# Performance work log

Hardware: AMD Instinct MI355X
Metric: run time of the kernel (lower is better)

## Reference

```python
import jax, jax.numpy as jnp
import numpy as np

DIM = 512
HEADS = 8
DIM_HEAD = 64
INNER = HEADS * DIM_HEAD
SCALE = DIM_HEAD ** -0.5


def setup_inputs() -> dict:
    key = jax.random.key(0)
    ks = jax.random.split(key, 6)
    b, n = 2, 2048
    x = jax.random.normal(ks[0], (b, n, DIM), dtype=jnp.float32)
    # torch Linear(dim, 3*inner, bias=False): store as [in, out] for x @ W
    w_qkv = jax.random.normal(ks[1], (DIM, 3 * INNER), dtype=jnp.float32) * (DIM ** -0.5)
    # Conv2d(heads, heads, 1, bias=False) weights squeezed to [out_h, in_h]
    w_pre = jax.random.normal(ks[2], (HEADS, HEADS), dtype=jnp.float32) * (HEADS ** -0.5)
    w_post = jax.random.normal(ks[3], (HEADS, HEADS), dtype=jnp.float32) * (HEADS ** -0.5)
    w_out = jax.random.normal(ks[4], (INNER, DIM), dtype=jnp.float32) * (INNER ** -0.5)
    b_out = jax.random.normal(ks[5], (DIM,), dtype=jnp.float32) * 0.01
    return {"x": x, "w_qkv": w_qkv, "w_pre": w_pre, "w_post": w_post,
            "w_out": w_out, "b_out": b_out}


def reference(x, w_qkv, w_pre, w_post, w_out, b_out):
    b, n, _ = x.shape
    qkv = x @ w_qkv  # [b, n, 3*inner]
    q, k, v = jnp.split(qkv, 3, axis=-1)
    # b n (h d) -> b h n d
    split_heads = lambda t: t.reshape(b, n, HEADS, DIM_HEAD).transpose(0, 2, 1, 3)
    q, k, v = split_heads(q), split_heads(k), split_heads(v)
    dots = jnp.einsum('bhid,bhjd->bhij', q, k) * SCALE
    # pre-softmax talking-heads: 1x1 conv over the head axis
    dots = jnp.einsum('gh,bhij->bgij', w_pre, dots)
    attn = jax.nn.softmax(dots, axis=-1)
    # post-softmax talking-heads mix
    attn = jnp.einsum('gh,bhij->bgij', w_post, attn)
    out = jnp.einsum('bhij,bhjd->bhid', attn, v)
    out = out.transpose(0, 2, 1, 3).reshape(b, n, INNER)  # b h n d -> b n (h d)
    return out @ w_out + b_out
```

## Files before the change

### kernel.cpp

```cpp
#include <hip/hip_runtime.h>
#include <hip/hip_bf16.h>

typedef unsigned short ushort_t;
typedef __attribute__((ext_vector_type(8))) short short8;
typedef __attribute__((ext_vector_type(4))) short short4v;
typedef __attribute__((ext_vector_type(4))) float floatx4;

#define MFMA16(a, b, c) __builtin_amdgcn_mfma_f32_16x16x32_bf16(a, b, c, 0, 0, 0)

__device__ __forceinline__ float bf2f(ushort_t u) {
    unsigned int v = ((unsigned int)u) << 16;
    return __int_as_float((int)v);
}
__device__ __forceinline__ ushort_t f2bf(float f) {
    unsigned int x = (unsigned int)__float_as_int(f);
    unsigned int r = (x + 0x7FFFu + ((x >> 16) & 1u)) >> 16;
    return (ushort_t)r;
}

__global__ __launch_bounds__(256) void k_cvt(const floatx4* __restrict__ src,
                                             short4v* __restrict__ dst, int n4) {
    int i = blockIdx.x * 256 + threadIdx.x;
    if (i < n4) {
        floatx4 v = src[i];
        short4v o;
        o[0] = (short)f2bf(v[0]);
        o[1] = (short)f2bf(v[1]);
        o[2] = (short)f2bf(v[2]);
        o[3] = (short)f2bf(v[3]);
        dst[i] = o;
    }
}

__global__ __launch_bounds__(256) void k_transpose_cvt(const float* __restrict__ src,
                                                       ushort_t* __restrict__ dst, int R, int C) {
    __shared__ float t[32][33];
    int tx = threadIdx.x & 31, ty = threadIdx.x >> 5;
    int r0 = blockIdx.y * 32, c0 = blockIdx.x * 32;
    for (int y = ty; y < 32; y += 8) t[y][tx] = src[(r0 + y) * C + c0 + tx];
    __syncthreads();
    for (int y = ty; y < 32; y += 8) dst[(c0 + y) * R + r0 + tx] = f2bf(t[tx][y]);
}

__global__ __launch_bounds__(256) void k_qkv(const ushort_t* __restrict__ x,
                                             const ushort_t* __restrict__ wt,
                                             ushort_t* __restrict__ qs,
                                             ushort_t* __restrict__ ks,
                                             ushort_t* __restrict__ vt) {
    __shared__ __align__(16) ushort_t st[64 * 72];
    const int tid = threadIdx.x, lane = tid & 63, wv = tid >> 6;
    const int col = lane & 15, quad = lane >> 4;
    const int row0 = blockIdx.y * 64 + (wv >> 1) * 32;
    const int c0 = blockIdx.x * 64 + (wv & 1) * 32;
    const int which = blockIdx.x >> 3, hh = blockIdx.x & 7;
    const int brow0 = blockIdx.y * 64;
    const int bb = brow0 >> 11, n0 = brow0 & 2047;
    const int hidx = bb * 8 + hh;
    floatx4 acc[2][2];
#pragma unroll
    for (int i = 0; i < 2; i++)
#pragma unroll
        for (int j = 0; j < 2; j++) acc[i][j] = (floatx4){0.f, 0.f, 0.f, 0.f};
    for (int k0 = 0; k0 < 512; k0 += 32) {
        const int ko = k0 + quad * 8;
        short8 a0 = *(const short8*)&x[(row0 + col) * 512 + ko];
        short8 a1 = *(const short8*)&x[(row0 + 16 + col) * 512 + ko];
        short8 b0 = *(const short8*)&wt[(c0 + col) * 512 + ko];
        short8 b1 = *(const short8*)&wt[(c0 + 16 + col) * 512 + ko];
        acc[0][0] = MFMA16(a0, b0, acc[0][0]);
        acc[0][1] = MFMA16(a0, b1, acc[0][1]);
        acc[1][0] = MFMA16(a1, b0, acc[1][0]);
        acc[1][1] = MFMA16(a1, b1, acc[1][1]);
    }
    const float qscale = (which == 0) ? 0.125f : 1.0f;
#pragma unroll
    for (int i = 0; i < 2; i++)
#pragma unroll
        for (int j = 0; j < 2; j++)
#pragma unroll
            for (int r = 0; r < 4; r++) {
                int il = (wv >> 1) * 32 + i * 16 + quad * 4 + r;
                int cl = (wv & 1) * 32 + j * 16 + col;
                ushort_t hv = f2bf(acc[i][j][r] * qscale);
                if (which == 2) st[cl * 72 + il] = hv;
                else            st[il * 72 + cl] = hv;
            }
    __syncthreads();
    if (which < 2) {
        ushort_t* dst = (which == 0) ? qs : ks;
#pragma unroll
        for (int s = tid; s < 512; s += 256) {
            int rr = s >> 3, dc = (s & 7) * 8;
            *(short8*)&dst[(hidx * 2048 + n0 + rr) * 64 + dc] = *(const short8*)&st[rr * 72 + dc];
        }
    } else {
#pragma unroll
        for (int s = tid; s < 512; s += 256) {
            int d = s >> 3, nc = (s & 7) * 8;
            *(short8*)&vt[(hidx * 64 + d) * 2048 + n0 + nc] = *(const short8*)&st[d * 72 + nc];
        }
    }
}

__global__ __launch_bounds__(512, 2) void k_attn(const ushort_t* __restrict__ qs,
                                                 const ushort_t* __restrict__ ks,
                                                 const ushort_t* __restrict__ vt,
                                                 const float* __restrict__ w_pre,
                                                 const float* __restrict__ w_post,
                                                 const ushort_t* __restrict__ wot,
                                                 const float* __restrict__ bias,
                                                 float* __restrict__ out) {
    __shared__ __align__(16) ushort_t qlds[8 * 16 * 72];
    __shared__ __align__(16) ushort_t U[8 * 16 * 136];
    __shared__ __align__(16) ushort_t oline[16 * 520];
    __shared__ float wbuf[128];
    __shared__ float lred[8][8][16];
    __shared__ float linv[8][16];
    const int tid = threadIdx.x, lane = tid & 63, wv = tid >> 6;
    const int col = lane & 15, quad = lane >> 4;
    const int b = blockIdx.y, n0 = blockIdx.x * 16;
    const int e = wv;

    if (tid < 64) wbuf[tid] = w_pre[tid];
    else if (tid < 128) wbuf[tid] = w_post[tid - 64];
    for (int c = tid; c < 1024; c += 512) {
        int hh = c >> 7, rem = c & 127, ii = rem >> 3, dc = (rem & 7) * 8;
        *(short8*)&qlds[(hh * 16 + ii) * 72 + dc] =
            *(const short8*)&qs[((b * 8 + hh) * 2048 + n0 + ii) * 64 + dc];
    }
    __syncthreads();

    float Lacc[8][4];
    floatx4 Oa[8][4];
#pragma unroll
    for (int g = 0; g < 8; g++) {
#pragma unroll
        for (int r = 0; r < 4; r++) Lacc[g][r] = 0.f;
#pragma unroll
        for (int nt = 0; nt < 4; nt++) Oa[g][nt] = (floatx4){0.f, 0.f, 0.f, 0.f};
    }

    for (int jt = 0; jt < 16; jt++) {
        const int j0 = jt * 128;
        const int jw = j0 + wv * 16;
        floatx4 S[8];
#pragma unroll
        for (int h = 0; h < 8; h++) {
            const ushort_t* qb = &qlds[(h * 16 + col) * 72 + quad * 8];
            short8 a0 = *(const short8*)&qb[0];
            short8 a1 = *(const short8*)&qb[32];
            const ushort_t* kb = &ks[((b * 8 + h) * 2048 + jw + col) * 64 + quad * 8];
            short8 b0 = *(const short8*)&kb[0];
            short8 b1 = *(const short8*)&kb[32];
            floatx4 a = (floatx4){0.f, 0.f, 0.f, 0.f};
            a = MFMA16(a0, b0, a);
            a = MFMA16(a1, b1, a);
            S[h] = a;
        }
#pragma unroll
        for (int g = 0; g < 8; g++)
#pragma unroll
            for (int r = 0; r < 4; r++) {
                float s = 0.f;
#pragma unroll
                for (int h = 0; h < 8; h++) s = fmaf(wbuf[g * 8 + h], S[h][r], s);
                float u = __expf(s);
                Lacc[g][r] += u;
                U[(g * 16 + quad * 4 + r) * 136 + wv * 16 + col] = f2bf(u);
            }
        __syncthreads();
#pragma unroll
        for (int k2 = 0; k2 < 4; k2++) {
            short8 bf[4];
#pragma unroll
            for (int nt = 0; nt < 4; nt++)
                bf[nt] = *(const short8*)&vt[((b * 8 + e) * 64 + nt * 16 + col) * 2048 + j0 +
                                             k2 * 32 + quad * 8];
            short8 af[8];
#pragma unroll
            for (int g = 0; g < 8; g++)
                af[g] = *(const short8*)&U[(g * 16 + col) * 136 + k2 * 32 + quad * 8];
#pragma unroll
            for (int g = 0; g < 8; g++)
#pragma unroll
                for (int nt = 0; nt < 4; nt++) Oa[g][nt] = MFMA16(af[g], bf[nt], Oa[g][nt]);
        }
        __syncthreads();
    }

#pragma unroll
    for (int g = 0; g < 8; g++)
#pragma unroll
        for (int r = 0; r < 4; r++) {
            float v = Lacc[g][r];
            v += __shfl_xor(v, 1, 64);
            v += __shfl_xor(v, 2, 64);
            v += __shfl_xor(v, 4, 64);
            v += __shfl_xor(v, 8, 64);
            if (col == 0) lred[wv][g][quad * 4 + r] = v;
        }
    __syncthreads();
    if (tid < 128) {
        int g = tid >> 4, ii = tid & 15;
        float l = 0.f;
#pragma unroll
        for (int w2 = 0; w2 < 8; w2++) l += lred[w2][g][ii];
        linv[g][ii] = 1.0f / l;
    }
    __syncthreads();
    float coef[8][4];
#pragma unroll
    for (int g = 0; g < 8; g++) {
        float wqe = wbuf[64 + e * 8 + g];
#pragma unroll
        for (int r = 0; r < 4; r++) coef[g][r] = wqe * linv[g][quad * 4 + r];
    }
#pragma unroll
    for (int nt = 0; nt < 4; nt++)
#pragma unroll
        for (int r = 0; r < 4; r++) {
            float o = 0.f;
#pragma unroll
            for (int g = 0; g < 8; g++) o = fmaf(coef[g][r], Oa[g][nt][r], o);
            oline[(quad * 4 + r) * 520 + e * 64 + nt * 16 + col] = f2bf(o);
        }
    __syncthreads();
#pragma unroll
    for (int nt = 0; nt < 4; nt++) {
        floatx4 acc = (floatx4){0.f, 0.f, 0.f, 0.f};
        const int c = wv * 64 + nt * 16 + col;
#pragma unroll
        for (int k2 = 0; k2 < 16; k2++) {
            short8 af = *(const short8*)&oline[col * 520 + k2 * 32 + quad * 8];
            short8 bf = *(const short8*)&wot[c * 512 + k2 * 32 + quad * 8];
            acc = MFMA16(af, bf, acc);
        }
        float bz = bias[c];
#pragma unroll
        for (int r = 0; r < 4; r++)
            out[(b * 2048 + n0 + quad * 4 + r) * 512 + c] = acc[r] + bz;
    }
}

extern "C" void kernel_launch(void* const* d_in, const int* in_sizes, int n_in,
                              void* d_out, int out_size, void* d_ws, size_t ws_size,
                              hipStream_t stream) {
    const float* x = (const float*)d_in[0];
    const float* w_qkv = (const float*)d_in[1];
    const float* w_pre = (const float*)d_in[2];
    const float* w_post = (const float*)d_in[3];
    const float* w_out = (const float*)d_in[4];
    const float* b_out = (const float*)d_in[5];
    char* ws = (char*)d_ws;
    ushort_t* qs = (ushort_t*)(ws);
    ushort_t* ks = (ushort_t*)(ws + (4u << 20));
    ushort_t* vt = (ushort_t*)(ws + (8u << 20));
    ushort_t* xb = (ushort_t*)(ws + (12u << 20));
    ushort_t* wt = (ushort_t*)(ws + (16u << 20));
    ushort_t* wot = (ushort_t*)(ws + (16u << 20) + 1572864u);
    float* out = (float*)d_out;

    k_cvt<<<dim3(2048), dim3(256), 0, stream>>>((const floatx4*)x, (short4v*)xb, 524288);
    k_transpose_cvt<<<dim3(48, 16), dim3(256), 0, stream>>>(w_qkv, wt, 512, 1536);
    k_transpose_cvt<<<dim3(16, 16), dim3(256), 0, stream>>>(w_out, wot, 512, 512);
    k_qkv<<<dim3(24, 64), dim3(256), 0, stream>>>(xb, wt, qs, ks, vt);
    k_attn<<<dim3(128, 2), dim3(512), 0, stream>>>(qs, ks, vt, w_pre, w_post, wot, b_out, out);
}
```

Measured before the change: 308.1 us.

## Double-buffer U tile and prefetch K/V into registers to overlap loads

```diff
diff --git a/kernel.cpp b/kernel.cpp
--- a/kernel.cpp
+++ b/kernel.cpp
@@ -16,6 +16,13 @@
     unsigned int x = (unsigned int)__float_as_int(f);
     unsigned int r = (x + 0x7FFFu + ((x >> 16) & 1u)) >> 16;
     return (ushort_t)r;
+}
+__device__ __forceinline__ floatx4 fma4(float a, floatx4 b, floatx4 c) {
+    c[0] = fmaf(a, b[0], c[0]);
+    c[1] = fmaf(a, b[1], c[1]);
+    c[2] = fmaf(a, b[2], c[2]);
+    c[3] = fmaf(a, b[3], c[3]);
+    return c;
 }
 
 __global__ __launch_bounds__(256) void k_cvt(const floatx4* __restrict__ src,
@@ -111,7 +118,7 @@
                                                  const float* __restrict__ bias,
                                                  float* __restrict__ out) {
     __shared__ __align__(16) ushort_t qlds[8 * 16 * 72];
-    __shared__ __align__(16) ushort_t U[8 * 16 * 136];
+    __shared__ __align__(16) ushort_t U[2][8 * 16 * 136];
     __shared__ __align__(16) ushort_t oline[16 * 520];
     __shared__ float wbuf[128];
     __shared__ float lred[8][8][16];
@@ -128,64 +135,92 @@
         *(short8*)&qlds[(hh * 16 + ii) * 72 + dc] =
             *(const short8*)&qs[((b * 8 + hh) * 2048 + n0 + ii) * 64 + dc];
     }
-    __syncthreads();
-
-    float Lacc[8][4];
+
+    floatx4 Lacc[8];
     floatx4 Oa[8][4];
 #pragma unroll
     for (int g = 0; g < 8; g++) {
-#pragma unroll
-        for (int r = 0; r < 4; r++) Lacc[g][r] = 0.f;
+        Lacc[g] = (floatx4){0.f, 0.f, 0.f, 0.f};
 #pragma unroll
         for (int nt = 0; nt < 4; nt++) Oa[g][nt] = (floatx4){0.f, 0.f, 0.f, 0.f};
     }
 
+    short8 kb0[8], kb1[8];
+    {
+        const int jw = wv * 16;
+#pragma unroll
+        for (int h = 0; h < 8; h++) {
+            const ushort_t* kp = &ks[((b * 8 + h) * 2048 + jw + col) * 64 + quad * 8];
+            kb0[h] = *(const short8*)&kp[0];
+            kb1[h] = *(const short8*)&kp[32];
+        }
+    }
+    __syncthreads();
+
+    int cur = 0;
     for (int jt = 0; jt < 16; jt++) {
-        const int j0 = jt * 128;
-        const int jw = j0 + wv * 16;
         floatx4 S[8];
 #pragma unroll
         for (int h = 0; h < 8; h++) {
             const ushort_t* qb = &qlds[(h * 16 + col) * 72 + quad * 8];
             short8 a0 = *(const short8*)&qb[0];
             short8 a1 = *(const short8*)&qb[32];
-            const ushort_t* kb = &ks[((b * 8 + h) * 2048 + jw + col) * 64 + quad * 8];
-            short8 b0 = *(const short8*)&kb[0];
-            short8 b1 = *(const short8*)&kb[32];
             floatx4 a = (floatx4){0.f, 0.f, 0.f, 0.f};
-            a = MFMA16(a0, b0, a);
-            a = MFMA16(a1, b1, a);
+            a = MFMA16(a0, kb0[h], a);
+            a = MFMA16(a1, kb1[h], a);
             S[h] = a;
         }
-#pragma unroll
-        for (int g = 0; g < 8; g++)
-#pragma unroll
-            for (int r = 0; r < 4; r++) {
-                float s = 0.f;
-#pragma unroll
-                for (int h = 0; h < 8; h++) s = fmaf(wbuf[g * 8 + h], S[h][r], s);
-                float u = __expf(s);
-                Lacc[g][r] += u;
-                U[(g * 16 + quad * 4 + r) * 136 + wv * 16 + col] = f2bf(u);
+        short8 vbr[16];
+        const int j0 = jt * 128;
+#pragma unroll
+        for (int k2 = 0; k2 < 4; k2++)
+#pragma unroll
+            for (int nt = 0; nt < 4; nt++)
+                vbr[k2 * 4 + nt] = *(const short8*)&vt[((b * 8 + e) * 64 + nt * 16 + col) * 2048 +
+                                                       j0 + k2 * 32 + quad * 8];
+        if (jt < 15) {
+            const int jw = (jt + 1) * 128 + wv * 16;
+#pragma unroll
+            for (int h = 0; h < 8; h++) {
+                const ushort_t* kp = &ks[((b * 8 + h) * 2048 + jw + col) * 64 + quad * 8];
+                kb0[h] = *(const short8*)&kp[0];
+                kb1[h] = *(const short8*)&kp[32];
             }
-        __syncthreads();
+        }
+        ushort_t* Uc = U[cur];
+#pragma unroll
+        for (int g = 0; g < 8; g++) {
+            floatx4 w0 = *(const floatx4*)&wbuf[g * 8];
+            floatx4 w1 = *(const floatx4*)&wbuf[g * 8 + 4];
+            floatx4 s4 = (floatx4){0.f, 0.f, 0.f, 0.f};
+#pragma unroll
+            for (int h = 0; h < 4; h++) s4 = fma4(w0[h], S[h], s4);
+#pragma unroll
+            for (int h = 0; h < 4; h++) s4 = fma4(w1[h], S[h + 4], s4);
+            floatx4 u4;
+            u4[0] = __expf(s4[0]);
+            u4[1] = __expf(s4[1]);
+            u4[2] = __expf(s4[2]);
+            u4[3] = __expf(s4[3]);
+            Lacc[g] += u4;
+#pragma unroll
+            for (int r = 0; r < 4; r++)
+                Uc[(g * 16 + quad * 4 + r) * 136 + wv * 16 + col] = f2bf(u4[r]);
+        }
+        asm volatile("s_waitcnt lgkmcnt(0)\n\ts_barrier" ::: "memory");
 #pragma unroll
         for (int k2 = 0; k2 < 4; k2++) {
-            short8 bf[4];
-#pragma unroll
-            for (int nt = 0; nt < 4; nt++)
-                bf[nt] = *(const short8*)&vt[((b * 8 + e) * 64 + nt * 16 + col) * 2048 + j0 +
-                                             k2 * 32 + quad * 8];
             short8 af[8];
 #pragma unroll
             for (int g = 0; g < 8; g++)
-                af[g] = *(const short8*)&U[(g * 16 + col) * 136 + k2 * 32 + quad * 8];
+                af[g] = *(const short8*)&Uc[(g * 16 + col) * 136 + k2 * 32 + quad * 8];
 #pragma unroll
             for (int g = 0; g < 8; g++)
 #pragma unroll
-                for (int nt = 0; nt < 4; nt++) Oa[g][nt] = MFMA16(af[g], bf[nt], Oa[g][nt]);
-        }
-        __syncthreads();
+                for (int nt = 0; nt < 4; nt++)
+                    Oa[g][nt] = MFMA16(af[g], vbr[k2 * 4 + nt], Oa[g][nt]);
+        }
+        cur ^= 1;
     }
 
 #pragma unroll
```

Result: slower. 510.8 us (+65.8%).
